# Optimization experiments

Hardware: AMD Instinct MI355X
Metric: run time of the kernel (lower is better)

The kernel has to match this reference:

```python
import jax, jax.numpy as jnp
import numpy as np

B, L_DEC, L_ENC = 4, 1024, 1024
D_MODEL, D_INNER, N_HEAD, D_K, D_V = 512, 256, 8, 64, 64
TEMP = D_K ** 0.5
EPS = 1e-6


def _layernorm(x, g, b):
    mu = jnp.mean(x, axis=-1, keepdims=True)
    var = jnp.mean(jnp.square(x - mu), axis=-1, keepdims=True)
    return (x - mu) * jax.lax.rsqrt(var + EPS) * g + b


def _mha(x_q, x_kv, Wq, Wk, Wv, Wfc, ln_g, ln_b, mask):
    # Faithful to source: only the query input is layer-normed; k/v use raw x_kv.
    resid = x_q
    qn = _layernorm(x_q, ln_g, ln_b)
    # Stacked per-head projections: Wq/Wk/Wv are [H, d_k, d_model]
    q = jnp.einsum('bld,hkd->bhlk', qn, Wq) / TEMP   # [B,H,Lq,dk]
    k = jnp.einsum('bld,hkd->bhlk', x_kv, Wk)        # [B,H,Lk,dk]
    v = jnp.einsum('bld,hkd->bhlk', x_kv, Wv)        # [B,H,Lk,dv]
    scores = jnp.einsum('bhqd,bhkd->bhqk', q, k)     # [B,H,Lq,Lk]
    if mask is not None:
        scores = jnp.where(mask[:, None, :, :] == 0, -jnp.inf, scores)
    attn = jax.nn.softmax(scores, axis=-1)
    out = jnp.einsum('bhqk,bhkd->bhqd', attn, v)     # [B,H,Lq,dv]
    Bq, H, Lq, dv = out.shape
    out = out.transpose(0, 2, 1, 3).reshape(Bq, Lq, H * dv)
    return out @ Wfc.T + resid


def _ffn(x, W1, b1, W2, b2, ln_g, ln_b):
    resid = x
    h = _layernorm(x, ln_g, ln_b)
    h = jax.nn.relu(h @ W1.T + b1) @ W2.T + b2
    return h + resid


def setup_inputs() -> dict:
    key = jax.random.key(0)
    ks = jax.random.split(key, 20)
    s = 0.02
    dec_input = jax.random.normal(ks[0], (B, L_DEC, D_MODEL), jnp.float32)
    enc_output = jax.random.normal(ks[1], (B, L_ENC, D_MODEL), jnp.float32)
    slf_attn_mask = jnp.tril(jnp.ones((1, L_DEC, L_DEC), jnp.int32))  # causal
    p = {}
    for i, pre in enumerate(['slf', 'enc']):
        base = 2 + i * 4
        p[f'{pre}_Wq'] = jax.random.normal(ks[base], (N_HEAD, D_K, D_MODEL), jnp.float32) * s
        p[f'{pre}_Wk'] = jax.random.normal(ks[base + 1], (N_HEAD, D_K, D_MODEL), jnp.float32) * s
        p[f'{pre}_Wv'] = jax.random.normal(ks[base + 2], (N_HEAD, D_V, D_MODEL), jnp.float32) * s
        p[f'{pre}_Wfc'] = jax.random.normal(ks[base + 3], (D_MODEL, N_HEAD * D_V), jnp.float32) * s
        p[f'{pre}_ln_g'] = jnp.ones((D_MODEL,), jnp.float32)
        p[f'{pre}_ln_b'] = jnp.zeros((D_MODEL,), jnp.float32)
    p['ffn_W1'] = jax.random.normal(ks[10], (D_INNER, D_MODEL), jnp.float32) * s
    p['ffn_b1'] = jnp.zeros((D_INNER,), jnp.float32)
    p['ffn_W2'] = jax.random.normal(ks[11], (D_MODEL, D_INNER), jnp.float32) * s
    p['ffn_b2'] = jnp.zeros((D_MODEL,), jnp.float32)
    p['ffn_ln_g'] = jnp.ones((D_MODEL,), jnp.float32)
    p['ffn_ln_b'] = jnp.zeros((D_MODEL,), jnp.float32)
    return {'dec_input': dec_input, 'enc_output': enc_output,
            'slf_attn_mask': slf_attn_mask, **p}


def reference(dec_input, enc_output,
              slf_Wq, slf_Wk, slf_Wv, slf_Wfc, slf_ln_g, slf_ln_b,
              enc_Wq, enc_Wk, enc_Wv, enc_Wfc, enc_ln_g, enc_ln_b,
              ffn_W1, ffn_b1, ffn_W2, ffn_b2, ffn_ln_g, ffn_ln_b,
              slf_attn_mask):
    x = _mha(dec_input, dec_input, slf_Wq, slf_Wk, slf_Wv, slf_Wfc,
             slf_ln_g, slf_ln_b, slf_attn_mask)
    x = _mha(x, enc_output, enc_Wq, enc_Wk, enc_Wv, enc_Wfc,
             enc_ln_g, enc_ln_b, None)
    x = _ffn(x, ffn_W1, ffn_b1, ffn_W2, ffn_b2, ffn_ln_g, ffn_ln_b)
    return x
```

## Files before the change

### kernel.cpp

```cpp
#include <hip/hip_runtime.h>
#include <hip/hip_bf16.h>
#include <math.h>

#define DMODEL 512
#define NHEAD  8
#define DHEAD  64

typedef __attribute__((ext_vector_type(8))) short bf16x8;
typedef __attribute__((ext_vector_type(4))) float f32x4;
typedef __attribute__((ext_vector_type(4))) short short4v;

static __device__ inline short f2bf(float f) {
    __hip_bfloat16 h = __float2bfloat16(f);
    return *reinterpret_cast<short*>(&h);
}

#define GLOAD_LDS16(gp, lp)                                                      \
    __builtin_amdgcn_global_load_lds(                                            \
        (const __attribute__((address_space(1))) unsigned int*)(gp),             \
        (__attribute__((address_space(3))) unsigned int*)(lp), 16, 0, 0)

struct CvtArgs {
    const float* src[12];
    short*       dst[12];
    int          n[12];
};

__global__ __launch_bounds__(256) void cvt_kernel(CvtArgs args) {
    int t = blockIdx.y;
    int idx = (blockIdx.x * 256 + threadIdx.x) * 8;
    if (idx >= args.n[t]) return;
    const float* s = args.src[t] + idx;
    float4 a = *(const float4*)s;
    float4 b = *(const float4*)(s + 4);
    bf16x8 o;
    o[0] = f2bf(a.x); o[1] = f2bf(a.y); o[2] = f2bf(a.z); o[3] = f2bf(a.w);
    o[4] = f2bf(b.x); o[5] = f2bf(b.y); o[6] = f2bf(b.z); o[7] = f2bf(b.w);
    *(bf16x8*)(args.dst[t] + idx) = o;
}

__global__ __launch_bounds__(256) void ln_kernel(const float* __restrict__ X,
                                                 const float* __restrict__ gam,
                                                 const float* __restrict__ bet,
                                                 short* __restrict__ Y) {
    int row = blockIdx.x * 4 + (threadIdx.x >> 6);
    int tid = threadIdx.x & 63;
    const float* x = X + (size_t)row * DMODEL;
    float4 a = *(const float4*)(x + tid * 4);
    float4 b = *(const float4*)(x + 256 + tid * 4);
    float sum = a.x + a.y + a.z + a.w + b.x + b.y + b.z + b.w;
    float sq  = a.x*a.x + a.y*a.y + a.z*a.z + a.w*a.w
              + b.x*b.x + b.y*b.y + b.z*b.z + b.w*b.w;
#pragma unroll
    for (int off = 1; off < 64; off <<= 1) {
        sum += __shfl_xor(sum, off);
        sq  += __shfl_xor(sq, off);
    }
    float mu  = sum * (1.0f / DMODEL);
    float var = sq * (1.0f / DMODEL) - mu * mu;
    float r   = rsqrtf(var + 1e-6f);

    float4 g1 = *(const float4*)(gam + tid * 4);
    float4 c1 = *(const float4*)(bet + tid * 4);
    float4 g2 = *(const float4*)(gam + 256 + tid * 4);
    float4 c2 = *(const float4*)(bet + 256 + tid * 4);
    short4v y1, y2;
    y1.x = f2bf((a.x - mu) * r * g1.x + c1.x);
    y1.y = f2bf((a.y - mu) * r * g1.y + c1.y);
    y1.z = f2bf((a.z - mu) * r * g1.z + c1.z);
    y1.w = f2bf((a.w - mu) * r * g1.w + c1.w);
    y2.x = f2bf((b.x - mu) * r * g2.x + c2.x);
    y2.y = f2bf((b.y - mu) * r * g2.y + c2.y);
    y2.z = f2bf((b.z - mu) * r * g2.z + c2.z);
    y2.w = f2bf((b.w - mu) * r * g2.w + c2.w);
    short* y = Y + (size_t)row * DMODEL;
    *(short4v*)(y + tid * 4)       = y1;
    *(short4v*)(y + 256 + tid * 4) = y2;
}

struct GJobs {
    const short* A[3];
    const short* W[3];
    const float* bias[3];
    const float* resid[3];
    void*        C[3];
    int M[3], N[3], K[3];
    float scale[3];
    int relu[3], obf[3], nblk[3];
};

__global__ __launch_bounds__(256) void gemm_bf16(GJobs jb) {
    __shared__ short As[2][64 * 64];
    __shared__ short Bs[2][64 * 64];

    int bid = blockIdx.x, j = 0;
    while (j < 2 && bid >= jb.nblk[j]) { bid -= jb.nblk[j]; ++j; }
    const short* __restrict__ A = jb.A[j];
    const short* __restrict__ W = jb.W[j];
    const int N = jb.N[j], K = jb.K[j];
    {
        int nb = jb.nblk[j];
        if ((nb & 7) == 0) bid = (bid & 7) * (nb >> 3) + (bid >> 3);
    }
    const int nbx = N >> 6;
    const int tn = (bid % nbx) * 64;
    const int tm = (bid / nbx) * 64;

    const int tid  = threadIdx.x;
    const int w    = tid >> 6;
    const int l    = tid & 63;
    const int lq   = l & 15;
    const int g    = l >> 4;
    const int wm   = (w >> 1) * 32;
    const int wn   = (w & 1) * 32;
    const int lrow = l >> 3;
    const int lsl  = l & 7;

    f32x4 acc[2][2];
#pragma unroll
    for (int i = 0; i < 2; ++i)
#pragma unroll
        for (int jj = 0; jj < 2; ++jj)
            acc[i][jj] = (f32x4){0.f, 0.f, 0.f, 0.f};

    const int nkt = K >> 6;

#pragma unroll
    for (int i = 0; i < 2; ++i) {
        int row = i * 32 + w * 8 + lrow;
        int slot = lsl ^ (row & 7);
        GLOAD_LDS16(A + (size_t)(tm + row) * K + slot * 8,
                    &As[0][i * 2048 + w * 512]);
        GLOAD_LDS16(W + (size_t)(tn + row) * K + slot * 8,
                    &Bs[0][i * 2048 + w * 512]);
    }

#pragma unroll 2
    for (int kt = 0; kt < nkt; ++kt) {
        const int cur = kt & 1;
        __syncthreads();
        if (kt + 1 < nkt) {
            const int k0n = (kt + 1) * 64;
#pragma unroll
            for (int i = 0; i < 2; ++i) {
                int row = i * 32 + w * 8 + lrow;
                int slot = lsl ^ (row & 7);
                GLOAD_LDS16(A + (size_t)(tm + row) * K + k0n + slot * 8,
                            &As[cur ^ 1][i * 2048 + w * 512]);
                GLOAD_LDS16(W + (size_t)(tn + row) * K + k0n + slot * 8,
                            &Bs[cur ^ 1][i * 2048 + w * 512]);
            }
        }

#pragma unroll
        for (int ks = 0; ks < 2; ++ks) {
            const int sl = ((ks * 4 + g) ^ (lq & 7)) * 8;
            bf16x8 af[2], bfv[2];
#pragma unroll
            for (int i = 0; i < 2; ++i) {
                af[i]  = *(const bf16x8*)&As[cur][(wm + i * 16 + lq) * 64 + sl];
                bfv[i] = *(const bf16x8*)&Bs[cur][(wn + i * 16 + lq) * 64 + sl];
            }
#pragma unroll
            for (int i = 0; i < 2; ++i)
#pragma unroll
                for (int jj = 0; jj < 2; ++jj)
                    acc[i][jj] = __builtin_amdgcn_mfma_f32_16x16x32_bf16(
                        af[i], bfv[jj], acc[i][jj], 0, 0, 0);
        }
    }

    const float* bias  = jb.bias[j];
    const float* resid = jb.resid[j];
    const float scale  = jb.scale[j];
    const int relu = jb.relu[j], obf = jb.obf[j];
#pragma unroll
    for (int i = 0; i < 2; ++i) {
#pragma unroll
        for (int r = 0; r < 4; ++r) {
            int row = tm + wm + i * 16 + g * 4 + r;
#pragma unroll
            for (int jj = 0; jj < 2; ++jj) {
                int col = tn + wn + jj * 16 + lq;
                float v = acc[i][jj][r] * scale;
                if (bias)  v += bias[col];
                if (resid) v += resid[(size_t)row * N + col];
                if (relu)  v = fmaxf(v, 0.f);
                if (obf) ((short*)jb.C[j])[(size_t)row * N + col] = f2bf(v);
                else     ((float*)jb.C[j])[(size_t)row * N + col] = v;
            }
        }
    }
}

__global__ __launch_bounds__(256) void attn_mfma_kernel(
        const short* __restrict__ Q, const short* __restrict__ K,
        const short* __restrict__ V, short* __restrict__ O,
        int Lq, int Lk, int causal, int qs, int kvs) {
    __shared__ short Kt[64 * 64];
    __shared__ short Vt[64][72];
    __shared__ short Pb[4][16][72];

    const int tid  = threadIdx.x;
    const int wave = tid >> 6;
    const int lane = tid & 63;
    const int lq   = lane & 15;
    const int g    = lane >> 4;
    const int bh   = blockIdx.y;
    const int b = bh >> 3, h = bh & 7;
    const int NQT = Lq >> 4;
    int gw = blockIdx.x * 4 + wave;
    const int qt = (gw & 1) ? (NQT - 1 - (gw >> 1)) : (gw >> 1);
    const int q0 = qt * 16;
    const float NEG = -__builtin_inff();

    size_t qoff = (size_t)(b * Lq + q0 + lq) * qs + h * DHEAD;
    bf16x8 qf0 = *(const bf16x8*)(Q + qoff + g * 8);
    bf16x8 qf1 = *(const bf16x8*)(Q + qoff + 32 + g * 8);

    f32x4 o[4] = {{0,0,0,0},{0,0,0,0},{0,0,0,0},{0,0,0,0}};
    f32x4 lacc = {0.f, 0.f, 0.f, 0.f};

    bf16x8 ones;
    {
        short ov = (lq == 0) ? (short)0x3F80 : (short)0;
#pragma unroll
        for (int i = 0; i < 8; ++i) ones[i] = ov;
    }

    const int nkt = causal ? ((qt >> 2) + 1) : (Lk >> 6);
    const int lrow = lane >> 3;
    const int lsl  = lane & 7;
    const int va = tid & 31;
    const int vd = (tid >> 5) * 8;

#pragma unroll 1
    for (int kt = 0; kt < nkt; ++kt) {
        __syncthreads();
#pragma unroll
        for (int i = 0; i < 2; ++i) {
            int row = i * 32 + wave * 8 + lrow;
            int slot = lsl ^ (row & 7);
            GLOAD_LDS16(K + (size_t)(b * Lk + kt * 64 + row) * kvs + h * DHEAD + slot * 8,
                        Kt + i * 2048 + wave * 512);
        }
        {
            size_t gb = (size_t)(b * Lk + kt * 64 + 2 * va) * kvs + h * DHEAD + vd;
            bf16x8 v0 = *(const bf16x8*)(V + gb);
            bf16x8 v1 = *(const bf16x8*)(V + gb + kvs);
#pragma unroll
            for (int i = 0; i < 8; ++i) {
                unsigned p = (unsigned short)v0[i] | ((unsigned)(unsigned short)v1[i] << 16);
                *(unsigned*)&Vt[vd + i][2 * va] = p;
            }
        }
        __syncthreads();

        f32x4 s[4];
#pragma unroll
        for (int sub = 0; sub < 4; ++sub) {
            int rr = sub * 16 + lq;
            const int sl0 = ((0 + g) ^ (lq & 7)) * 8;
            const int sl1 = ((4 + g) ^ (lq & 7)) * 8;
            bf16x8 kf0 = *(const bf16x8*)&Kt[rr * 64 + sl0];
            bf16x8 kf1 = *(const bf16x8*)&Kt[rr * 64 + sl1];
            f32x4 a = {0.f, 0.f, 0.f, 0.f};
            a = __builtin_amdgcn_mfma_f32_16x16x32_bf16(kf0, qf0, a, 0, 0, 0);
            a = __builtin_amdgcn_mfma_f32_16x16x32_bf16(kf1, qf1, a, 0, 0, 0);
            s[sub] = a;
        }
        if (causal && kt == nkt - 1) {
            int qg = q0 + lq;
#pragma unroll
            for (int sub = 0; sub < 4; ++sub) {
#pragma unroll
                for (int r = 0; r < 4; ++r) {
                    int kg = kt * 64 + sub * 16 + g * 4 + r;
                    if (kg > qg) s[sub][r] = NEG;
                }
            }
        }

#pragma unroll
        for (int sub = 0; sub < 4; ++sub) {
            short4v p4;
            p4.x = f2bf(__expf(fminf(s[sub][0], 60.f)));
            p4.y = f2bf(__expf(fminf(s[sub][1], 60.f)));
            p4.z = f2bf(__expf(fminf(s[sub][2], 60.f)));
            p4.w = f2bf(__expf(fminf(s[sub][3], 60.f)));
            *(short4v*)&Pb[wave][lq][sub * 16 + g * 4] = p4;
        }
        bf16x8 pf0 = *(const bf16x8*)&Pb[wave][lq][g * 8];
        bf16x8 pf1 = *(const bf16x8*)&Pb[wave][lq][32 + g * 8];

#pragma unroll
        for (int dc = 0; dc < 4; ++dc) {
            bf16x8 vf0 = *(const bf16x8*)&Vt[dc * 16 + lq][g * 8];
            bf16x8 vf1 = *(const bf16x8*)&Vt[dc * 16 + lq][32 + g * 8];
            o[dc] = __builtin_amdgcn_mfma_f32_16x16x32_bf16(pf0, vf0, o[dc], 0, 0, 0);
            o[dc] = __builtin_amdgcn_mfma_f32_16x16x32_bf16(pf1, vf1, o[dc], 0, 0, 0);
        }
        lacc = __builtin_amdgcn_mfma_f32_16x16x32_bf16(pf0, ones, lacc, 0, 0, 0);
        lacc = __builtin_amdgcn_mfma_f32_16x16x32_bf16(pf1, ones, lacc, 0, 0, 0);
    }

#pragma unroll
    for (int r = 0; r < 4; ++r) {
        float lr = __shfl(lacc[r], g << 4);
        float inv = 1.f / lr;
        size_t ob = (size_t)(b * Lq + q0 + g * 4 + r) * qs + h * DHEAD + lq;
        O[ob + 0]  = f2bf(o[0][r] * inv);
        O[ob + 16] = f2bf(o[1][r] * inv);
        O[ob + 32] = f2bf(o[2][r] * inv);
        O[ob + 48] = f2bf(o[3][r] * inv);
    }
}

static void launch_gemm(GJobs& jb, int njobs, hipStream_t stream) {
    int total = 0;
    for (int i = 0; i < 3; ++i) { if (i >= njobs) jb.nblk[i] = 0; total += jb.nblk[i]; }
    gemm_bf16<<<total, 256, 0, stream>>>(jb);
}

extern "C" void kernel_launch(void* const* d_in, const int* in_sizes, int n_in,
                              void* d_out, int out_size, void* d_ws, size_t ws_size,
                              hipStream_t stream) {
    const float* dec       = (const float*)d_in[0];
    const float* enc       = (const float*)d_in[1];
    const float* slf_Wq    = (const float*)d_in[3];
    const float* slf_Wk    = (const float*)d_in[4];
    const float* slf_Wv    = (const float*)d_in[5];
    const float* slf_Wfc   = (const float*)d_in[6];
    const float* slf_ln_g  = (const float*)d_in[7];
    const float* slf_ln_b  = (const float*)d_in[8];
    const float* enc_Wq    = (const float*)d_in[9];
    const float* enc_Wk    = (const float*)d_in[10];
    const float* enc_Wv    = (const float*)d_in[11];
    const float* enc_Wfc   = (const float*)d_in[12];
    const float* enc_ln_g  = (const float*)d_in[13];
    const float* enc_ln_b  = (const float*)d_in[14];
    const float* ffn_W1    = (const float*)d_in[15];
    const float* ffn_b1    = (const float*)d_in[16];
    const float* ffn_W2    = (const float*)d_in[17];
    const float* ffn_b2    = (const float*)d_in[18];
    const float* ffn_ln_g  = (const float*)d_in[19];
    const float* ffn_ln_b  = (const float*)d_in[20];
    float* out = (float*)d_out;

    const int Bb = 4, L = 1024, M = Bb * L;
    const size_t NE = (size_t)M * DMODEL;
    const int WQN = NHEAD * DHEAD * DMODEL;
    float* ws = (float*)d_ws;
    float* x1 = ws;
    float* x2 = ws + NE;
    short* kv16e = (short*)x2;
    short* sb = (short*)(ws + 2 * NE);
    short* dec16 = sb;               sb += NE;
    short* enc16 = sb;               sb += NE;
    short* qn16  = sb;               sb += NE;
    short* q16   = sb;               sb += NE;
    short* ao16  = sb;               sb += NE;
    short* kv16  = sb;               sb += 2 * NE;
    short* h16   = sb;               sb += NE / 2;
    short* wq_s  = sb;               sb += WQN;
    short* wkv_s = sb;               sb += 2 * WQN;
    short* wfc_s = sb;               sb += WQN;
    short* wq_e  = sb;               sb += WQN;
    short* wkv_e = sb;               sb += 2 * WQN;
    short* wfc_e = sb;               sb += WQN;
    short* w1_16 = sb;               sb += 256 * DMODEL;
    short* w2_16 = sb;               sb += DMODEL * 256;

    CvtArgs ca;
    ca.src[0] = dec;     ca.dst[0] = dec16;         ca.n[0] = (int)NE;
    ca.src[1] = enc;     ca.dst[1] = enc16;         ca.n[1] = (int)NE;
    ca.src[2] = slf_Wq;  ca.dst[2] = wq_s;          ca.n[2] = WQN;
    ca.src[3] = slf_Wk;  ca.dst[3] = wkv_s;         ca.n[3] = WQN;
    ca.src[4] = slf_Wv;  ca.dst[4] = wkv_s + WQN;   ca.n[4] = WQN;
    ca.src[5] = slf_Wfc; ca.dst[5] = wfc_s;         ca.n[5] = WQN;
    ca.src[6] = enc_Wq;  ca.dst[6] = wq_e;          ca.n[6] = WQN;
    ca.src[7] = enc_Wk;  ca.dst[7] = wkv_e;         ca.n[7] = WQN;
    ca.src[8] = enc_Wv;  ca.dst[8] = wkv_e + WQN;   ca.n[8] = WQN;
    ca.src[9] = enc_Wfc; ca.dst[9] = wfc_e;         ca.n[9] = WQN;
    ca.src[10] = ffn_W1; ca.dst[10] = w1_16;        ca.n[10] = 256 * DMODEL;
    ca.src[11] = ffn_W2; ca.dst[11] = w2_16;        ca.n[11] = DMODEL * 256;
    cvt_kernel<<<dim3(1024, 12), 256, 0, stream>>>(ca);

    dim3 attn_grid(L / 64, Bb * NHEAD);
    const int NB512  = (M / 64) * (512 / 64);
    const int NB1024 = (M / 64) * (1024 / 64);
    const int NB256  = (M / 64) * (256 / 64);

    ln_kernel<<<M / 4, 256, 0, stream>>>(dec, slf_ln_g, slf_ln_b, qn16);
    {
        GJobs jb = {};
        jb.A[0] = qn16;  jb.W[0] = wq_s;  jb.C[0] = q16;
        jb.M[0] = M; jb.N[0] = 512;  jb.K[0] = 512; jb.scale[0] = 0.125f;
        jb.obf[0] = 1; jb.nblk[0] = NB512;
        jb.A[1] = dec16; jb.W[1] = wkv_s; jb.C[1] = kv16;
        jb.M[1] = M; jb.N[1] = 1024; jb.K[1] = 512; jb.scale[1] = 1.f;
        jb.obf[1] = 1; jb.nblk[1] = NB1024;
        jb.A[2] = enc16; jb.W[2] = wkv_e; jb.C[2] = kv16e;
        jb.M[2] = M; jb.N[2] = 1024; jb.K[2] = 512; jb.scale[2] = 1.f;
        jb.obf[2] = 1; jb.nblk[2] = NB1024;
        launch_gemm(jb, 3, stream);
    }
    attn_mfma_kernel<<<attn_grid, 256, 0, stream>>>(q16, kv16, kv16 + 512, ao16,
                                                    L, L, 1, DMODEL, 1024);
    {
        GJobs jb = {};
        jb.A[0] = ao16; jb.W[0] = wfc_s; jb.resid[0] = dec; jb.C[0] = x1;
        jb.M[0] = M; jb.N[0] = 512; jb.K[0] = 512; jb.scale[0] = 1.f;
        jb.obf[0] = 0; jb.nblk[0] = NB512;
        launch_gemm(jb, 1, stream);
    }

    ln_kernel<<<M / 4, 256, 0, stream>>>(x1, enc_ln_g, enc_ln_b, qn16);
    {
        GJobs jb = {};
        jb.A[0] = qn16; jb.W[0] = wq_e; jb.C[0] = q16;
        jb.M[0] = M; jb.N[0] = 512; jb.K[0] = 512; jb.scale[0] = 0.125f;
        jb.obf[0] = 1; jb.nblk[0] = NB512;
        launch_gemm(jb, 1, stream);
    }
    attn_mfma_kernel<<<attn_grid, 256, 0, stream>>>(q16, kv16e, kv16e + 512, ao16,
                                                    L, L, 0, DMODEL, 1024);
    {
        GJobs jb = {};
        jb.A[0] = ao16; jb.W[0] = wfc_e; jb.resid[0] = x1; jb.C[0] = x2;
        jb.M[0] = M; jb.N[0] = 512; jb.K[0] = 512; jb.scale[0] = 1.f;
        jb.obf[0] = 0; jb.nblk[0] = NB512;
        launch_gemm(jb, 1, stream);
    }

    ln_kernel<<<M / 4, 256, 0, stream>>>(x2, ffn_ln_g, ffn_ln_b, qn16);
    {
        GJobs jb = {};
        jb.A[0] = qn16; jb.W[0] = w1_16; jb.bias[0] = ffn_b1; jb.C[0] = h16;
        jb.M[0] = M; jb.N[0] = 256; jb.K[0] = 512; jb.scale[0] = 1.f;
        jb.relu[0] = 1; jb.obf[0] = 1; jb.nblk[0] = NB256;
        launch_gemm(jb, 1, stream);
    }
    {
        GJobs jb = {};
        jb.A[0] = h16; jb.W[0] = w2_16; jb.bias[0] = ffn_b2; jb.resid[0] = x2;
        jb.C[0] = out;
        jb.M[0] = M; jb.N[0] = 512; jb.K[0] = 256; jb.scale[0] = 1.f;
        jb.obf[0] = 0; jb.nblk[0] = NB512;
        launch_gemm(jb, 1, stream);
    }
}
```

Before: 243.6 us.

## Split attention over key ranges with a combine pass; compact cvt grid

```diff
diff --git a/kernel.cpp b/kernel.cpp
--- a/kernel.cpp
+++ b/kernel.cpp
@@ -24,11 +24,14 @@
     const float* src[12];
     short*       dst[12];
     int          n[12];
+    int          start[12];
 };
 
 __global__ __launch_bounds__(256) void cvt_kernel(CvtArgs args) {
-    int t = blockIdx.y;
-    int idx = (blockIdx.x * 256 + threadIdx.x) * 8;
+    int bid = blockIdx.x;
+    int t = 0;
+    while (t < 11 && bid >= args.start[t + 1]) ++t;
+    int idx = ((bid - args.start[t]) * 256 + threadIdx.x) * 8;
     if (idx >= args.n[t]) return;
     const float* s = args.src[t] + idx;
     float4 a = *(const float4*)s;
@@ -195,8 +198,9 @@
 
 __global__ __launch_bounds__(256) void attn_mfma_kernel(
         const short* __restrict__ Q, const short* __restrict__ K,
-        const short* __restrict__ V, short* __restrict__ O,
-        int Lq, int Lk, int causal, int qs, int kvs) {
+        const short* __restrict__ V, float* __restrict__ Opart,
+        float* __restrict__ Lpart,
+        int Lq, int Lk, int causal, int qs, int kvs, int S) {
     __shared__ short Kt[64 * 64];
     __shared__ short Vt[64][72];
     __shared__ short Pb[4][16][72];
@@ -208,10 +212,8 @@
     const int g    = lane >> 4;
     const int bh   = blockIdx.y;
     const int b = bh >> 3, h = bh & 7;
-    const int NQT = Lq >> 4;
-    int gw = blockIdx.x * 4 + wave;
-    const int qt = (gw & 1) ? (NQT - 1 - (gw >> 1)) : (gw >> 1);
-    const int q0 = qt * 16;
+    const int sp = blockIdx.z;
+    const int q0 = blockIdx.x * 64 + wave * 16;
     const float NEG = -__builtin_inff();
 
     size_t qoff = (size_t)(b * Lq + q0 + lq) * qs + h * DHEAD;
@@ -228,14 +230,16 @@
         for (int i = 0; i < 8; ++i) ones[i] = ov;
     }
 
-    const int nkt = causal ? ((qt >> 2) + 1) : (Lk >> 6);
+    const int nkt = causal ? (blockIdx.x + 1) : (Lk >> 6);
+    const int klo = (sp * nkt) / S;
+    const int khi = ((sp + 1) * nkt) / S;
     const int lrow = lane >> 3;
     const int lsl  = lane & 7;
     const int va = tid & 31;
     const int vd = (tid >> 5) * 8;
 
 #pragma unroll 1
-    for (int kt = 0; kt < nkt; ++kt) {
+    for (int kt = klo; kt < khi; ++kt) {
         __syncthreads();
 #pragma unroll
         for (int i = 0; i < 2; ++i) {
@@ -304,16 +308,45 @@
         lacc = __builtin_amdgcn_mfma_f32_16x16x32_bf16(pf1, ones, lacc, 0, 0, 0);
     }
 
+    float* opw = Opart + ((size_t)(sp * 32 + bh) * Lq + q0) * 64;
 #pragma unroll
     for (int r = 0; r < 4; ++r) {
-        float lr = __shfl(lacc[r], g << 4);
-        float inv = 1.f / lr;
-        size_t ob = (size_t)(b * Lq + q0 + g * 4 + r) * qs + h * DHEAD + lq;
-        O[ob + 0]  = f2bf(o[0][r] * inv);
-        O[ob + 16] = f2bf(o[1][r] * inv);
-        O[ob + 32] = f2bf(o[2][r] * inv);
-        O[ob + 48] = f2bf(o[3][r] * inv);
-    }
+        int row = g * 4 + r;
+        opw[(size_t)row * 64 + lq]      = o[0][r];
+        opw[(size_t)row * 64 + 16 + lq] = o[1][r];
+        opw[(size_t)row * 64 + 32 + lq] = o[2][r];
+        opw[(size_t)row * 64 + 48 + lq] = o[3][r];
+        if (lq == 0)
+            Lpart[(size_t)(sp * 32 + bh) * Lq + q0 + row] = lacc[r];
+    }
+}
+
+__global__ __launch_bounds__(256) void attn_combine(
+        const float* __restrict__ Opart, const float* __restrict__ Lpart,
+        short* __restrict__ O, int S) {
+    const int BH = 32, L = 1024;
+    int t  = blockIdx.x * 256 + threadIdx.x;
+    int d8 = (t & 7) * 8;
+    int q  = (t >> 3) & (L - 1);
+    int bh = t >> 13;
+    int b = bh >> 3, hd = bh & 7;
+    f32x4 a0 = {0.f, 0.f, 0.f, 0.f}, a1 = {0.f, 0.f, 0.f, 0.f};
+    float l = 0.f;
+    for (int sp = 0; sp < S; ++sp) {
+        const float* p = Opart + (((size_t)sp * BH + bh) * L + q) * 64 + d8;
+        a0 += *(const f32x4*)p;
+        a1 += *(const f32x4*)(p + 4);
+        l  += Lpart[((size_t)sp * BH + bh) * L + q];
+    }
+    float inv = 1.f / l;
+    short* o = O + ((size_t)(b * L + q)) * DMODEL + hd * DHEAD + d8;
+    short4v y0, y1;
+    y0.x = f2bf(a0[0] * inv); y0.y = f2bf(a0[1] * inv);
+    y0.z = f2bf(a0[2] * inv); y0.w = f2bf(a0[3] * inv);
+    y1.x = f2bf(a1[0] * inv); y1.y = f2bf(a1[1] * inv);
+    y1.z = f2bf(a1[2] * inv); y1.w = f2bf(a1[3] * inv);
+    *(short4v*)o       = y0;
+    *(short4v*)(o + 4) = y1;
 }
 
 static void launch_gemm(GJobs& jb, int njobs, hipStream_t stream) {
@@ -371,6 +404,14 @@
     short* w1_16 = sb;               sb += 256 * DMODEL;
     short* w2_16 = sb;               sb += DMODEL * 256;
 
+    size_t used = (size_t)((char*)sb - (char*)d_ws);
+    used = (used + 255) & ~(size_t)255;
+    const size_t per_split = (size_t)32 * L * 64 * 4 + (size_t)32 * L * 4;
+    int S = 1;
+    if (ws_size >= used + 2 * per_split) S = 2;
+    float* Opart = (float*)((char*)d_ws + used);
+    float* Lpart = Opart + (size_t)S * 32 * L * 64;
+
     CvtArgs ca;
     ca.src[0] = dec;     ca.dst[0] = dec16;         ca.n[0] = (int)NE;
     ca.src[1] = enc;     ca.dst[1] = enc16;         ca.n[1] = (int)NE;
@@ -384,9 +425,14 @@
     ca.src[9] = enc_Wfc; ca.dst[9] = wfc_e;         ca.n[9] = WQN;
     ca.src[10] = ffn_W1; ca.dst[10] = w1_16;        ca.n[10] = 256 * DMODEL;
     ca.src[11] = ffn_W2; ca.dst[11] = w2_16;        ca.n[11] = DMODEL * 256;
-    cvt_kernel<<<dim3(1024, 12), 256, 0, stream>>>(ca);
-
-    dim3 attn_grid(L / 64, Bb * NHEAD);
+    {
+        int acc = 0;
+        for (int t = 0; t < 12; ++t) { ca.start[t] = acc; acc += ca.n[t] / 2048; }
+        cvt_kernel<<<acc, 256, 0, stream>>>(ca);
+    }
+
+    dim3 attn_grid(L / 64, Bb * NHEAD, S);
+    const int ncomb = (32 * L * 8) / 256;
     const int NB512  = (M / 64) * (512 / 64);
     const int NB1024 = (M / 64) * (1024 / 64);
     const int NB256  = (M / 64) * (256 / 64);
@@ -405,8 +451,10 @@
         jb.obf[2] = 1; jb.nblk[2] = NB1024;
         launch_gemm(jb, 3, stream);
     }
-    attn_mfma_kernel<<<attn_grid, 256, 0, stream>>>(q16, kv16, kv16 + 512, ao16,
-                                                    L, L, 1, DMODEL, 1024);
+    attn_mfma_kernel<<<attn_grid, 256, 0, stream>>>(q16, kv16, kv16 + 512,
+                                                    Opart, Lpart, L, L, 1,
+                                                    DMODEL, 1024, S);
+    attn_combine<<<ncomb, 256, 0, stream>>>(Opart, Lpart, ao16, S);
     {
         GJobs jb = {};
         jb.A[0] = ao16; jb.W[0] = wfc_s; jb.resid[0] = dec; jb.C[0] = x1;
@@ -423,8 +471,10 @@
         jb.obf[0] = 1; jb.nblk[0] = NB512;
         launch_gemm(jb, 1, stream);
     }
-    attn_mfma_kernel<<<attn_grid, 256, 0, stream>>>(q16, kv16e, kv16e + 512, ao16,
-                                                    L, L, 0, DMODEL, 1024);
+    attn_mfma_kernel<<<attn_grid, 256, 0, stream>>>(q16, kv16e, kv16e + 512,
+                                                    Opart, Lpart, L, L, 0,
+                                                    DMODEL, 1024, S);
+    attn_combine<<<ncomb, 256, 0, stream>>>(Opart, Lpart, ao16, S);
     {
         GJobs jb = {};
         jb.A[0] = ao16; jb.W[0] = wfc_e; jb.resid[0] = x1; jb.C[0] = x2;
```

Result: slower. 251.9 us (+3.4%).

## Split attention KV tiles across two wave groups and compact convert grid

Applied to the files above, without the earlier changes.

```diff
diff --git a/kernel.cpp b/kernel.cpp
--- a/kernel.cpp
+++ b/kernel.cpp
@@ -24,11 +24,14 @@
     const float* src[12];
     short*       dst[12];
     int          n[12];
+    int          start[12];
 };
 
 __global__ __launch_bounds__(256) void cvt_kernel(CvtArgs args) {
-    int t = blockIdx.y;
-    int idx = (blockIdx.x * 256 + threadIdx.x) * 8;
+    int bid = blockIdx.x;
+    int t = 0;
+    while (t < 11 && bid >= args.start[t + 1]) ++t;
+    int idx = ((bid - args.start[t]) * 256 + threadIdx.x) * 8;
     if (idx >= args.n[t]) return;
     const float* s = args.src[t] + idx;
     float4 a = *(const float4*)s;
@@ -193,25 +196,25 @@
     }
 }
 
-__global__ __launch_bounds__(256) void attn_mfma_kernel(
+__global__ __launch_bounds__(512) void attn_mfma_kernel(
         const short* __restrict__ Q, const short* __restrict__ K,
         const short* __restrict__ V, short* __restrict__ O,
         int Lq, int Lk, int causal, int qs, int kvs) {
-    __shared__ short Kt[64 * 64];
-    __shared__ short Vt[64][72];
-    __shared__ short Pb[4][16][72];
+    __shared__ short Kt[2][64 * 64];
+    __shared__ short Vt[2][64][72];
+    __shared__ short Pb[8][16][72];
 
     const int tid  = threadIdx.x;
     const int wave = tid >> 6;
+    const int wq4  = wave & 3;
+    const int tsel = wave >> 2;
     const int lane = tid & 63;
     const int lq   = lane & 15;
     const int g    = lane >> 4;
     const int bh   = blockIdx.y;
     const int b = bh >> 3, h = bh & 7;
-    const int NQT = Lq >> 4;
-    int gw = blockIdx.x * 4 + wave;
-    const int qt = (gw & 1) ? (NQT - 1 - (gw >> 1)) : (gw >> 1);
-    const int q0 = qt * 16;
+    const int qx = causal ? ((int)gridDim.x - 1 - (int)blockIdx.x) : (int)blockIdx.x;
+    const int q0 = qx * 64 + wq4 * 16;
     const float NEG = -__builtin_inff();
 
     size_t qoff = (size_t)(b * Lq + q0 + lq) * qs + h * DHEAD;
@@ -228,33 +231,38 @@
         for (int i = 0; i < 8; ++i) ones[i] = ov;
     }
 
-    const int nkt = causal ? ((qt >> 2) + 1) : (Lk >> 6);
+    const int nkt = causal ? (qx + 1) : (Lk >> 6);
+    const int npair = (nkt + 1) >> 1;
     const int lrow = lane >> 3;
     const int lsl  = lane & 7;
-    const int va = tid & 31;
-    const int vd = (tid >> 5) * 8;
+    const int gt = tid & 255;
+    const int va = gt & 31;
+    const int vd = (gt >> 5) * 8;
 
 #pragma unroll 1
-    for (int kt = 0; kt < nkt; ++kt) {
+    for (int kp = 0; kp < npair; ++kp) {
+        const int t = 2 * kp + tsel;
+        const int active = (t < nkt);
         __syncthreads();
-#pragma unroll
-        for (int i = 0; i < 2; ++i) {
-            int row = i * 32 + wave * 8 + lrow;
-            int slot = lsl ^ (row & 7);
-            GLOAD_LDS16(K + (size_t)(b * Lk + kt * 64 + row) * kvs + h * DHEAD + slot * 8,
-                        Kt + i * 2048 + wave * 512);
-        }
-        {
-            size_t gb = (size_t)(b * Lk + kt * 64 + 2 * va) * kvs + h * DHEAD + vd;
+        if (active) {
+#pragma unroll
+            for (int i = 0; i < 2; ++i) {
+                int row = i * 32 + wq4 * 8 + lrow;
+                int slot = lsl ^ (row & 7);
+                GLOAD_LDS16(K + (size_t)(b * Lk + t * 64 + row) * kvs + h * DHEAD + slot * 8,
+                            &Kt[tsel][i * 2048 + wq4 * 512]);
+            }
+            size_t gb = (size_t)(b * Lk + t * 64 + 2 * va) * kvs + h * DHEAD + vd;
             bf16x8 v0 = *(const bf16x8*)(V + gb);
             bf16x8 v1 = *(const bf16x8*)(V + gb + kvs);
 #pragma unroll
             for (int i = 0; i < 8; ++i) {
                 unsigned p = (unsigned short)v0[i] | ((unsigned)(unsigned short)v1[i] << 16);
-                *(unsigned*)&Vt[vd + i][2 * va] = p;
+                *(unsigned*)&Vt[tsel][vd + i][2 * va] = p;
             }
         }
         __syncthreads();
+        if (!active) continue;
 
         f32x4 s[4];
 #pragma unroll
@@ -262,20 +270,20 @@
             int rr = sub * 16 + lq;
             const int sl0 = ((0 + g) ^ (lq & 7)) * 8;
             const int sl1 = ((4 + g) ^ (lq & 7)) * 8;
-            bf16x8 kf0 = *(const bf16x8*)&Kt[rr * 64 + sl0];
-            bf16x8 kf1 = *(const bf16x8*)&Kt[rr * 64 + sl1];
+            bf16x8 kf0 = *(const bf16x8*)&Kt[tsel][rr * 64 + sl0];
+            bf16x8 kf1 = *(const bf16x8*)&Kt[tsel][rr * 64 + sl1];
             f32x4 a = {0.f, 0.f, 0.f, 0.f};
             a = __builtin_amdgcn_mfma_f32_16x16x32_bf16(kf0, qf0, a, 0, 0, 0);
             a = __builtin_amdgcn_mfma_f32_16x16x32_bf16(kf1, qf1, a, 0, 0, 0);
             s[sub] = a;
         }
-        if (causal && kt == nkt - 1) {
+        if (causal && t == nkt - 1) {
             int qg = q0 + lq;
 #pragma unroll
             for (int sub = 0; sub < 4; ++sub) {
 #pragma unroll
                 for (int r = 0; r < 4; ++r) {
-                    int kg = kt * 64 + sub * 16 + g * 4 + r;
+                    int kg = t * 64 + sub * 16 + g * 4 + r;
                     if (kg > qg) s[sub][r] = NEG;
                 }
             }
@@ -295,8 +303,8 @@
 
 #pragma unroll
         for (int dc = 0; dc < 4; ++dc) {
-            bf16x8 vf0 = *(const bf16x8*)&Vt[dc * 16 + lq][g * 8];
-            bf16x8 vf1 = *(const bf16x8*)&Vt[dc * 16 + lq][32 + g * 8];
+            bf16x8 vf0 = *(const bf16x8*)&Vt[tsel][dc * 16 + lq][g * 8];
+            bf16x8 vf1 = *(const bf16x8*)&Vt[tsel][dc * 16 + lq][32 + g * 8];
             o[dc] = __builtin_amdgcn_mfma_f32_16x16x32_bf16(pf0, vf0, o[dc], 0, 0, 0);
             o[dc] = __builtin_amdgcn_mfma_f32_16x16x32_bf16(pf1, vf1, o[dc], 0, 0, 0);
         }
@@ -304,15 +312,35 @@
         lacc = __builtin_amdgcn_mfma_f32_16x16x32_bf16(pf1, ones, lacc, 0, 0, 0);
     }
 
-#pragma unroll
-    for (int r = 0; r < 4; ++r) {
-        float lr = __shfl(lacc[r], g << 4);
-        float inv = 1.f / lr;
-        size_t ob = (size_t)(b * Lq + q0 + g * 4 + r) * qs + h * DHEAD + lq;
-        O[ob + 0]  = f2bf(o[0][r] * inv);
-        O[ob + 16] = f2bf(o[1][r] * inv);
-        O[ob + 32] = f2bf(o[2][r] * inv);
-        O[ob + 48] = f2bf(o[3][r] * inv);
+    float* Ox = (float*)&Pb[0][0][0];
+    float* Lx = Ox + 4 * 16 * 64;
+    __syncthreads();
+    if (tsel == 1) {
+#pragma unroll
+        for (int r = 0; r < 4; ++r) {
+            int row = g * 4 + r;
+            float* dst = Ox + (wq4 * 16 + row) * 64;
+            dst[lq]      = o[0][r];
+            dst[16 + lq] = o[1][r];
+            dst[32 + lq] = o[2][r];
+            dst[48 + lq] = o[3][r];
+            if (lq == 0) Lx[wq4 * 16 + row] = lacc[r];
+        }
+    }
+    __syncthreads();
+    if (tsel == 0) {
+#pragma unroll
+        for (int r = 0; r < 4; ++r) {
+            int row = g * 4 + r;
+            float lr = __shfl(lacc[r], g << 4) + Lx[wq4 * 16 + row];
+            float inv = 1.f / lr;
+            const float* srcx = Ox + (wq4 * 16 + row) * 64;
+            size_t ob = (size_t)(b * Lq + q0 + row) * qs + h * DHEAD + lq;
+            O[ob + 0]  = f2bf((o[0][r] + srcx[lq])      * inv);
+            O[ob + 16] = f2bf((o[1][r] + srcx[16 + lq]) * inv);
+            O[ob + 32] = f2bf((o[2][r] + srcx[32 + lq]) * inv);
+            O[ob + 48] = f2bf((o[3][r] + srcx[48 + lq]) * inv);
+        }
     }
 }
 
@@ -384,7 +412,11 @@
     ca.src[9] = enc_Wfc; ca.dst[9] = wfc_e;         ca.n[9] = WQN;
     ca.src[10] = ffn_W1; ca.dst[10] = w1_16;        ca.n[10] = 256 * DMODEL;
     ca.src[11] = ffn_W2; ca.dst[11] = w2_16;        ca.n[11] = DMODEL * 256;
-    cvt_kernel<<<dim3(1024, 12), 256, 0, stream>>>(ca);
+    {
+        int acc = 0;
+        for (int t = 0; t < 12; ++t) { ca.start[t] = acc; acc += ca.n[t] / 2048; }
+        cvt_kernel<<<acc, 256, 0, stream>>>(ca);
+    }
 
     dim3 attn_grid(L / 64, Bb * NHEAD);
     const int NB512  = (M / 64) * (512 / 64);
@@ -405,7 +437,7 @@
         jb.obf[2] = 1; jb.nblk[2] = NB1024;
         launch_gemm(jb, 3, stream);
     }
-    attn_mfma_kernel<<<attn_grid, 256, 0, stream>>>(q16, kv16, kv16 + 512, ao16,
+    attn_mfma_kernel<<<attn_grid, 512, 0, stream>>>(q16, kv16, kv16 + 512, ao16,
                                                     L, L, 1, DMODEL, 1024);
     {
         GJobs jb = {};
@@ -423,7 +455,7 @@
         jb.obf[0] = 1; jb.nblk[0] = NB512;
         launch_gemm(jb, 1, stream);
     }
-    attn_mfma_kernel<<<attn_grid, 256, 0, stream>>>(q16, kv16e, kv16e + 512, ao16,
+    attn_mfma_kernel<<<attn_grid, 512, 0, stream>>>(q16, kv16e, kv16e + 512, ao16,
                                                     L, L, 0, DMODEL, 1024);
     {
         GJobs jb = {};
```

Measured after the change: 238.6 us. 2.0% less time.
